# Kernel tuning notes

Hardware: AMD Instinct MI355X
Metric: run time of the kernel (lower is better)

Reference implementation:

```python
import jax, jax.numpy as jnp
import numpy as np

NEG_SLOPE = 0.01

def lrelu(x):
    return jax.nn.leaky_relu(x, NEG_SLOPE)

def lin(x, w, b):
    # torch Linear: x @ W.T + b, W shape (out, in)
    return x @ w.T + b

def meansum_pool(mask, x_local, *x_global):
    # masked sum + mean over points, concat with global/context vectors
    x_sum = (x_local * mask).sum(axis=1)                 # (b, d)
    x_mean = x_sum / mask.sum(axis=1)                    # (b, d) / (b, 1)
    return jnp.concatenate([x_mean, x_sum, *x_global], axis=1)


def setup_inputs() -> dict:
    key = jax.random.key(0)
    ks = jax.random.split(key, 16)
    B, N, DIN, DC, H, G, NB, DOUT = 16, 8192, 3, 16, 128, 10, 6, 3

    def w(k, shape, fan_in):
        return (jax.random.normal(k, shape, jnp.float32) / np.float32(np.sqrt(fan_in)))

    inp = {
        "x_local": jax.random.normal(ks[0], (B, N, DIN), jnp.float32),
        "context": jax.random.normal(ks[1], (B, DC), jnp.float32),
        "mask": (jax.random.uniform(ks[2], (B, N, 1)) < 0.9).astype(jnp.float32),
        # EPiC_Projection params (effective weight-normed weights)
        "proj_lw": w(ks[3], (H, DIN), DIN), "proj_lb": jnp.zeros((H,), jnp.float32),
        "proj_g0w": w(ks[4], (H, 2 * H + DC), 2 * H + DC), "proj_g0b": jnp.zeros((H,), jnp.float32),
        "proj_g1w": w(ks[5], (H, H), H), "proj_g1b": jnp.zeros((H,), jnp.float32),
        "proj_g2w": w(ks[6], (G, H), H), "proj_g2b": jnp.zeros((G,), jnp.float32),
        # stacked per-block EPiC_layer params
        "g1w": w(ks[7], (NB, H, 2 * H + G + DC), 2 * H + G + DC), "g1b": jnp.zeros((NB, H), jnp.float32),
        "g2w": w(ks[8], (NB, G, H), H), "g2b": jnp.zeros((NB, G), jnp.float32),
        "l1w": w(ks[9], (NB, H, H + G + DC), H + G + DC), "l1b": jnp.zeros((NB, H), jnp.float32),
        "l2w": w(ks[10], (NB, H, H), H), "l2b": jnp.zeros((NB, H), jnp.float32),
        # output head
        "outw": w(ks[11], (DOUT, H), H), "outb": jnp.zeros((DOUT,), jnp.float32),
    }
    return inp


def reference(x_local, context, mask,
              proj_lw, proj_lb, proj_g0w, proj_g0b, proj_g1w, proj_g1b, proj_g2w, proj_g2b,
              g1w, g1b, g2w, g2b, l1w, l1b, l2w, l2b, outw, outb):
    B, N, _ = x_local.shape
    # --- EPiC_Projection ---
    xl = lrelu(lin(x_local, proj_lw, proj_lb))           # (b, n, H)
    xg = meansum_pool(mask, xl, context)                 # (b, 2H + DC)
    xg = lrelu(lin(xg, proj_g0w, proj_g0b))
    xg = lrelu(lin(xg, proj_g1w, proj_g1b))
    xg = lrelu(lin(xg, proj_g2w, proj_g2b))              # (b, G)
    xl = xl * mask
    # --- EPiC layers (no skip: use_skip_connection=False -> +0) ---
    num_blocks = g1w.shape[0]
    for i in range(num_blocks):
        pooled = meansum_pool(mask, xl, xg, context)     # (b, 2H + G + DC)
        h_g = lrelu(lin(pooled, g1w[i], g1b[i]))
        xg = lrelu(lin(h_g, g2w[i], g2b[i]) + xg)        # residual global
        xg_b = jnp.broadcast_to(xg[:, None, :], (B, N, xg.shape[-1]))
        ctx_b = jnp.broadcast_to(context[:, None, :], (B, N, context.shape[-1]))
        cat = jnp.concatenate([xl, xg_b, ctx_b], axis=2)  # (b, n, H + G + DC)
        h_l = lrelu(lin(cat, l1w[i], l1b[i]))
        xl = lrelu(lin(h_l, l2w[i], l2b[i]) + xl) * mask  # residual local, masked
    h = lin(xl, outw, outb)                              # (b, n, 3)
    return h * mask
```

## Files before the change

kernel.cpp:

```cpp
#include <hip/hip_runtime.h>
#include <hip/hip_bf16.h>


typedef __attribute__((ext_vector_type(8))) short short8;
typedef __attribute__((ext_vector_type(4))) float f32x4;

#define B_ 16
#define N_ 8192
#define DC_ 16
#define H_ 128
#define G_ 10
#define NB_ 6
#define NEG_ 0.01f

__device__ __forceinline__ float lrelu(float x) { return x > 0.f ? x : NEG_ * x; }

__device__ __forceinline__ unsigned short f2bf(float x) {
  union { float f; unsigned u; } v; v.f = x;
  return (unsigned short)((v.u + 0x7fffu + ((v.u >> 16) & 1u)) >> 16);
}
__device__ __forceinline__ float bf2f(unsigned short u) {
  union { unsigned u; float f; } v; v.u = ((unsigned)u) << 16; return v.f;
}
__device__ __forceinline__ void split_bf(float x, unsigned short& h, unsigned short& l) {
  union { float f; unsigned u; } v; v.f = x;
  unsigned hu = v.u & 0xffff0000u;
  h = (unsigned short)(hu >> 16);
  union { unsigned u; float f; } hv; hv.u = hu;
  l = f2bf(x - hv.f);
}

__device__ __forceinline__ f32x4 mfma16(short8 a, short8 b, f32x4 c) {
  return __builtin_amdgcn_mfma_f32_16x16x32_bf16(a, b, c, 0, 0, 0);
}

__device__ __forceinline__ void make_frags(f32x4 v0, f32x4 v1, short8& bh, short8& bl) {
  unsigned short h, l;
#pragma unroll
  for (int j = 0; j < 4; ++j) {
    split_bf(v0[j], h, l);
    bh[j] = (short)h; bl[j] = (short)l;
  }
#pragma unroll
  for (int j = 0; j < 4; ++j) {
    split_bf(v1[j], h, l);
    bh[4 + j] = (short)h; bl[4 + j] = (short)l;
  }
}

__device__ __forceinline__ void async_cp16(const void* g, void* l) {
  __builtin_amdgcn_global_load_lds(
      (const __attribute__((address_space(1))) void*)g,
      (__attribute__((address_space(3))) void*)l, 16, 0, 0);
}

__device__ __forceinline__ void agent_store(float* p, float v) {
  __hip_atomic_store(p, v, __ATOMIC_RELAXED, __HIP_MEMORY_SCOPE_AGENT);
}
__device__ __forceinline__ float agent_load(const float* p) {
  return __hip_atomic_load(p, __ATOMIC_RELAXED, __HIP_MEMORY_SCOPE_AGENT);
}

template <int NS>
__device__ void epic_global_tail(
    int b, int tid, const float* __restrict__ pP, float cnt,
    const float* __restrict__ xg_cur, float* __restrict__ xg_next,
    const float* __restrict__ context,
    const float* __restrict__ g1w_n, const float* __restrict__ g1b_n,
    const float* __restrict__ g2w_n, const float* __restrict__ g2b_n,
    const float* __restrict__ l1w_n, const float* __restrict__ l1b_n,
    float* __restrict__ gbias_out, float* shx) {
  if (tid < 256) {
    const int f = tid & 127, kh = tid >> 7;
    const float* pr = pP + ((size_t)b * NS + kh * (NS / 2)) * 128 + f;
    float s = 0.f;
#pragma unroll 8
    for (int w = 0; w < NS / 2; ++w) s += agent_load(pr + w * 128);
    shx[tid] = s;
  }
  __syncthreads();
  if (tid < 128) {
    float s = shx[tid] + shx[tid + 128];
    shx[384 + tid] = s;
    shx[256 + tid] = s / cnt;
  }
  if (tid < G_) shx[512 + tid] = xg_cur[tid];
  if (tid >= 32 && tid < 32 + DC_) shx[522 + tid - 32] = context[b * DC_ + tid - 32];
  __syncthreads();
  if (tid < 256) {
    const int f = tid & 127, kh = tid >> 7;
    const float* wr = g1w_n + (size_t)f * 282 + kh * 142;
    const float* vp = shx + 256 + kh * 142;
    const int n2 = kh ? 70 : 71;
    float a = 0.f;
#pragma unroll 8
    for (int j = 0; j < n2; ++j) {
      float2 w2 = *(const float2*)(wr + 2 * j);
      a += w2.x * vp[2 * j] + w2.y * vp[2 * j + 1];
    }
    shx[tid] = a;
  }
  __syncthreads();
  if (tid < 128) shx[544 + tid] = lrelu(shx[tid] + shx[tid + 128] + g1b_n[tid]);
  __syncthreads();
  if (tid < G_) {
    const float* wr = g2w_n + tid * 128;
    float a = g2b_n[tid] + shx[512 + tid];
#pragma unroll 8
    for (int j = 0; j < 32; ++j) {
      float4 w4 = *(const float4*)(wr + 4 * j);
      a += w4.x * shx[544 + 4 * j] + w4.y * shx[544 + 4 * j + 1] +
           w4.z * shx[544 + 4 * j + 2] + w4.w * shx[544 + 4 * j + 3];
    }
    float v = lrelu(a);
    shx[672 + tid] = v;
    xg_next[tid] = v;
  }
  __syncthreads();
  if (tid < 128) {
    const float* wr = l1w_n + tid * 154;
    float a = l1b_n[tid];
#pragma unroll
    for (int j = 0; j < G_; ++j) a += wr[128 + j] * shx[672 + j];
#pragma unroll
    for (int j = 0; j < DC_; ++j) a += wr[138 + j] * shx[522 + j];
    gbias_out[tid] = a;
  }
}

__global__ __launch_bounds__(256) void prep_weights(
    const float* __restrict__ l1w, const float* __restrict__ l2w,
    unsigned short* __restrict__ w1h, unsigned short* __restrict__ w1l,
    unsigned short* __restrict__ w2h, unsigned short* __restrict__ w2l,
    unsigned int* __restrict__ counters) {
  int idx = blockIdx.x * 256 + threadIdx.x;
  const int total = NB_ * H_ * H_;
  if (idx < 112) counters[idx] = 0u;
  if (idx < total) {
    int i = idx / (H_ * H_), rem = idx % (H_ * H_);
    int F = rem / H_, k = rem % H_;
    int ks = k >> 5, c = k & 31;
    int mt2 = F >> 4, r2 = F & 15;
    int mt1 = ((F >> 5) << 1) | ((F >> 2) & 1);
    int r1 = (((F >> 3) & 3) << 2) | (F & 3);
    int off1 = i * 16384 + (mt1 * 4 + ks) * 512 + ((c >> 3) * 16 + r1) * 8 + (c & 7);
    int off2 = i * 16384 + (mt2 * 4 + ks) * 512 + ((c >> 3) * 16 + r2) * 8 + (c & 7);
    unsigned short h, l;
    split_bf(l1w[(i * H_ + F) * 154 + k], h, l);
    w1h[off1] = h; w1l[off1] = l;
    split_bf(l2w[(i * H_ + F) * H_ + k], h, l);
    w2h[off2] = h; w2l[off2] = l;
  }
}

__global__ __launch_bounds__(256, 2) void proj_local_kernel(
    const float* __restrict__ xloc, const float* __restrict__ maskp,
    const float* __restrict__ plw, const float* __restrict__ plb,
    float* __restrict__ xlf, float* __restrict__ pP,
    float* __restrict__ cntp, float* __restrict__ cnt_g,
    unsigned int* __restrict__ counters,
    const float* __restrict__ context,
    const float* __restrict__ g0w, const float* __restrict__ g0b,
    const float* __restrict__ g1pw, const float* __restrict__ g1pb,
    const float* __restrict__ g2pw, const float* __restrict__ g2pb,
    float* __restrict__ xg_g,
    const float* __restrict__ g1w0, const float* __restrict__ g1b0,
    const float* __restrict__ g2w0, const float* __restrict__ g2b0,
    const float* __restrict__ l1w0, const float* __restrict__ l1b0,
    float* __restrict__ gbias_g) {
  __shared__ float wq[H_][4];
  __shared__ float wsum[512];
  __shared__ float cw[4];
  __shared__ float shx[768];
  __shared__ int winflag;
  const int tid = threadIdx.x, bid = blockIdx.x;
  const int wv = tid >> 6, lane = tid & 63;
  const int q = lane >> 4, n16 = lane & 15;
  const int b = bid >> 6;
  if (tid < H_) {
    wq[tid][0] = plw[tid * 3 + 0];
    wq[tid][1] = plw[tid * 3 + 1];
    wq[tid][2] = plw[tid * 3 + 2];
    wq[tid][3] = plb[tid];
  }
  __syncthreads();
  const int t = bid * 4 + wv;
  const int p0 = t * 32;
  const int pa = p0 + n16, pb = p0 + 16 + n16;
  const float xa0 = xloc[pa * 3], xa1 = xloc[pa * 3 + 1], xa2 = xloc[pa * 3 + 2];
  const float xb0 = xloc[pb * 3], xb1 = xloc[pb * 3 + 1], xb2 = xloc[pb * 3 + 2];
  const float m0 = maskp[pa], m1 = maskp[pb];
  float* ga = xlf + (size_t)(2 * t) * 2048;
  float* gb = ga + 2048;
#pragma unroll
  for (int ms = 0; ms < 8; ++ms) {
    f32x4 v0, v1;
#pragma unroll
    for (int r = 0; r < 4; ++r) {
      const int F = ms * 16 + q * 4 + r;
      float4 w4 = *(const float4*)wq[F];
      v0[r] = lrelu(w4.x * xa0 + w4.y * xa1 + w4.z * xa2 + w4.w) * m0;
      v1[r] = lrelu(w4.x * xb0 + w4.y * xb1 + w4.z * xb2 + w4.w) * m1;
    }
    *(f32x4*)(ga + ms * 256 + (q * 16 + n16) * 4) = v0;
    *(f32x4*)(gb + ms * 256 + (q * 16 + n16) * 4) = v1;
    f32x4 s = v0 + v1;
#pragma unroll
    for (int r = 0; r < 4; ++r) {
      float sv = s[r];
      sv += __shfl_xor(sv, 1, 64);
      sv += __shfl_xor(sv, 2, 64);
      sv += __shfl_xor(sv, 4, 64);
      sv += __shfl_xor(sv, 8, 64);
      s[r] = sv;
    }
    if (n16 == 0) *(f32x4*)&wsum[wv * 128 + ms * 16 + q * 4] = s;
  }
  {
    float c = (q == 0) ? (m0 + m1) : 0.f;
    c += __shfl_xor(c, 1, 64);
    c += __shfl_xor(c, 2, 64);
    c += __shfl_xor(c, 4, 64);
    c += __shfl_xor(c, 8, 64);
    if (lane == 0) cw[wv] = c;
  }
  __syncthreads();
  if (tid < 128) {
    agent_store(&pP[(size_t)(2 * bid) * 128 + tid], wsum[tid] + wsum[128 + tid]);
    agent_store(&pP[(size_t)(2 * bid + 1) * 128 + tid], wsum[256 + tid] + wsum[384 + tid]);
  }
  if (tid == 0) agent_store(&cntp[bid], cw[0] + cw[1] + cw[2] + cw[3]);

  __syncthreads();
  if (tid == 0) winflag = (atomicAdd(&counters[b], 1u) == 63u) ? 1 : 0;
  __syncthreads();
  if (!winflag) return;
  if (tid < 64) shx[688 + tid] = agent_load(&cntp[b * 64 + tid]);
  __syncthreads();
  if (tid == 0) {
    float c = 0.f;
#pragma unroll
    for (int w = 0; w < 64; ++w) c += shx[688 + w];
    shx[752] = c;
    cnt_g[b] = c;
  }
  __syncthreads();
  const float cnt = shx[752];
  {
    const int f = tid & 127, kh = tid >> 7;
    const float* pr = pP + ((size_t)b * 128 + kh * 64) * 128 + f;
    float s = 0.f;
#pragma unroll 8
    for (int w = 0; w < 64; ++w) s += agent_load(pr + w * 128);
    shx[tid] = s;
  }
  __syncthreads();
  if (tid < 128) {
    float s = shx[tid] + shx[tid + 128];
    shx[384 + tid] = s;
    shx[256 + tid] = s / cnt;
  }
  if (tid < DC_) shx[512 + tid] = context[b * DC_ + tid];
  __syncthreads();
  {
    const int f = tid & 127, kh = tid >> 7;
    const float* wr = g0w + (size_t)f * 272 + kh * 136;
    const float* vp = shx + 256 + kh * 136;
    float a = 0.f;
#pragma unroll 8
    for (int j = 0; j < 34; ++j) {
      float4 w4 = *(const float4*)(wr + 4 * j);
      a += w4.x * vp[4 * j] + w4.y * vp[4 * j + 1] + w4.z * vp[4 * j + 2] + w4.w * vp[4 * j + 3];
    }
    __syncthreads();
    shx[tid] = a;
  }
  __syncthreads();
  if (tid < 128) shx[544 + tid] = lrelu(shx[tid] + shx[tid + 128] + g0b[tid]);
  __syncthreads();
  {
    const int f = tid & 127, kh = tid >> 7;
    const float* wr = g1pw + (size_t)f * 128 + kh * 64;
    const float* vp = shx + 544 + kh * 64;
    float a = 0.f;
#pragma unroll 8
    for (int j = 0; j < 16; ++j) {
      float4 w4 = *(const float4*)(wr + 4 * j);
      a += w4.x * vp[4 * j] + w4.y * vp[4 * j + 1] + w4.z * vp[4 * j + 2] + w4.w * vp[4 * j + 3];
    }
    __syncthreads();
    shx[tid] = a;
  }
  __syncthreads();
  if (tid < 128) shx[544 + tid] = lrelu(shx[tid] + shx[tid + 128] + g1pb[tid]);
  __syncthreads();
  if (tid < G_) {
    const float* wr = g2pw + tid * 128;
    float a = g2pb[tid];
#pragma unroll 8
    for (int j = 0; j < 32; ++j) {
      float4 w4 = *(const float4*)(wr + 4 * j);
      a += w4.x * shx[544 + 4 * j] + w4.y * shx[544 + 4 * j + 1] +
           w4.z * shx[544 + 4 * j + 2] + w4.w * shx[544 + 4 * j + 3];
    }
    xg_g[(0 * 16 + b) * 16 + tid] = lrelu(a);
  }
  __syncthreads();
  epic_global_tail<128>(b, tid, pP, cnt,
                        xg_g + (0 * 16 + b) * 16, xg_g + (1 * 16 + b) * 16, context,
                        g1w0, g1b0, g2w0, g2b0, l1w0, l1b0,
                        gbias_g + (size_t)(0 * 16 + b) * 128, shx);
}

__device__ __forceinline__ void load_frags(const float* base_g, int q, int n16,
                                           short8* xbh, short8* xbl) {
#pragma unroll
  for (int ks = 0; ks < 4; ++ks) {
    const float* pb = base_g + (2 * ks + (q >> 1)) * 256 + ((q & 1) * 32 + n16) * 4;
    f32x4 v0 = *(const f32x4*)pb;
    f32x4 v1 = *(const f32x4*)(pb + 64);
    make_frags(v0, v1, xbh[ks], xbl[ks]);
  }
}

template <bool LAST>
__device__ __forceinline__ void epic_pass(
    int g, int wv, int q, int n16, int lane16,
    const short8* xbh, const short8* xbl,
    const unsigned short* w1h_l, const unsigned short* w1l_l,
    const unsigned short* w2h_l, const unsigned short* w2l_l,
    const float* gbias_s, const float* l2b_s, const float* outw_s,
    float* wsum, float* __restrict__ xlf, const float* __restrict__ maskp,
    float* __restrict__ outp) {
  f32x4 acc2[8];
#pragma unroll
  for (int ms = 0; ms < 8; ++ms) acc2[ms] = (f32x4){0.f, 0.f, 0.f, 0.f};

#pragma unroll 1
  for (int ko = 0; ko < 4; ++ko) {
    f32x4 acc[2][2];
#pragma unroll
    for (int t = 0; t < 2; ++t)
#pragma unroll
      for (int kc = 0; kc < 2; ++kc) acc[t][kc] = (f32x4){0.f, 0.f, 0.f, 0.f};
#pragma unroll
    for (int t = 0; t < 2; ++t) {
#pragma unroll
      for (int kc = 0; kc < 2; ++kc) {
        short8 a1h[2], a1l[2];
#pragma unroll
        for (int u = 0; u < 2; ++u) {
          const int off = ((ko * 2 + t) * 4 + kc * 2 + u) * 512 + lane16;
          a1h[u] = *(const short8*)(w1h_l + off);
          a1l[u] = *(const short8*)(w1l_l + off);
        }
#pragma unroll
        for (int u = 0; u < 2; ++u) {
          const int ks = kc * 2 + u;
          acc[t][kc] = mfma16(a1h[u], xbh[ks], acc[t][kc]);
          acc[t][kc] = mfma16(a1l[u], xbh[ks], acc[t][kc]);
          acc[t][kc] = mfma16(a1h[u], xbl[ks], acc[t][kc]);
        }
      }
    }
    f32x4 gb0 = *(const f32x4*)&gbias_s[ko * 32 + q * 8];
    f32x4 gb1 = *(const f32x4*)&gbias_s[ko * 32 + q * 8 + 4];
    f32x4 hv0, hv1;
#pragma unroll
    for (int r = 0; r < 4; ++r) {
      hv0[r] = lrelu(acc[0][0][r] + acc[0][1][r] + gb0[r]);
      hv1[r] = lrelu(acc[1][0][r] + acc[1][1][r] + gb1[r]);
    }
    short8 b2h, b2l;
    make_frags(hv0, hv1, b2h, b2l);
#pragma unroll
    for (int mc = 0; mc < 4; ++mc) {
      short8 a2h[2], a2l[2];
#pragma unroll
      for (int u = 0; u < 2; ++u) {
        const int off = ((mc * 2 + u) * 4 + ko) * 512 + lane16;
        a2h[u] = *(const short8*)(w2h_l + off);
        a2l[u] = *(const short8*)(w2l_l + off);
      }
#pragma unroll
      for (int u = 0; u < 2; ++u) {
        const int ms = mc * 2 + u;
        acc2[ms] = mfma16(a2h[u], b2h, acc2[ms]);
        acc2[ms] = mfma16(a2l[u], b2h, acc2[ms]);
        acc2[ms] = mfma16(a2h[u], b2l, acc2[ms]);
      }
    }
  }

  const float mk = maskp[g * 16 + n16];
  float po[3];
  if (LAST) po[0] = po[1] = po[2] = 0.f;
  float* base_w = xlf + (size_t)g * 2048;
#pragma unroll
  for (int ms = 0; ms < 8; ++ms) {
    f32x4 lb4 = *(const f32x4*)&l2b_s[ms * 16 + q * 4];
    float* xo = base_w + ms * 256 + (q * 16 + n16) * 4;
    f32x4 old = *(const f32x4*)xo;
    f32x4 v;
#pragma unroll
    for (int r = 0; r < 4; ++r) v[r] = lrelu(acc2[ms][r] + lb4[r] + old[r]) * mk;
    if (!LAST) {
      *(f32x4*)xo = v;
      f32x4 sr;
#pragma unroll
      for (int r = 0; r < 4; ++r) {
        float s = v[r];
        s += __shfl_xor(s, 1, 64);
        s += __shfl_xor(s, 2, 64);
        s += __shfl_xor(s, 4, 64);
        s += __shfl_xor(s, 8, 64);
        sr[r] = s;
      }
      if (n16 == 0) *(f32x4*)&wsum[wv * 128 + ms * 16 + q * 4] = sr;
    } else {
      f32x4 w0 = *(const f32x4*)&outw_s[0 * 128 + ms * 16 + q * 4];
      f32x4 w1 = *(const f32x4*)&outw_s[1 * 128 + ms * 16 + q * 4];
      f32x4 w2 = *(const f32x4*)&outw_s[2 * 128 + ms * 16 + q * 4];
#pragma unroll
      for (int r = 0; r < 4; ++r) {
        po[0] += v[r] * w0[r];
        po[1] += v[r] * w1[r];
        po[2] += v[r] * w2[r];
      }
    }
  }
  if (LAST) {
#pragma unroll
    for (int o = 0; o < 3; ++o) {
      float s = po[o];
      s += __shfl_xor(s, 16, 64);
      s += __shfl_xor(s, 32, 64);
      po[o] = s;
    }
    if (q == 0) {
      const int p = g * 16 + n16;
#pragma unroll
      for (int o = 0; o < 3; ++o)
        outp[(size_t)p * 3 + o] = (po[o] + outw_s[384 + o]) * mk;
    }
  }
}

__global__ __launch_bounds__(1024) void epic_local_kernel(
    float* __restrict__ xlf, float* __restrict__ pP,
    const float* __restrict__ cnt_g, unsigned int* __restrict__ counters_blk,
    const float* __restrict__ gbias_in,
    const float* __restrict__ xg_tail_cur, float* __restrict__ xg_tail_next,
    float* __restrict__ gbias_tail_out,
    const float* __restrict__ context,
    const float* __restrict__ g1w_n, const float* __restrict__ g1b_n,
    const float* __restrict__ g2w_n, const float* __restrict__ g2b_n,
    const float* __restrict__ l1w_n, const float* __restrict__ l1b_n,
    const float* __restrict__ l2b,
    const unsigned short* __restrict__ w1h, const unsigned short* __restrict__ w1l,
    const unsigned short* __restrict__ w2h, const unsigned short* __restrict__ w2l,
    const float* __restrict__ maskp,
    float* __restrict__ outp) {
  __shared__ unsigned short wbuf[65536];
  __shared__ float shx[768];
  __shared__ float gbias_s[128];
  __shared__ float l2b_s[128];
  __shared__ float wsum[2048];
  __shared__ int winflag;
  const int tid = threadIdx.x, bid = blockIdx.x;
  const int b = bid >> 4;
  const int wv = tid >> 6, lane = tid & 63;
  const int q = lane >> 4, n16 = lane & 15;

  {
    const unsigned short* src =
        (wv < 4) ? w1h : (wv < 8) ? w1l : (wv < 12) ? w2h : w2l;
    const char* s8 = (const char*)(src + (wv & 3) * 4096) + lane * 16;
    char* d8 = (char*)wbuf + wv * 8192;
#pragma unroll
    for (int j = 0; j < 8; ++j) async_cp16(s8 + j * 1024, d8 + j * 1024);
  }
  if (tid < 128) {
    gbias_s[tid] = gbias_in[b * 128 + tid];
    l2b_s[tid] = l2b[tid];
  }

  const int gA = bid * 32 + wv;
  const int gB = bid * 32 + 16 + wv;
  short8 xbh[4], xbl[4];
  load_frags(xlf + (size_t)gA * 2048, q, n16, xbh, xbl);
  __syncthreads();

  const unsigned short* w1h_l = wbuf;
  const unsigned short* w1l_l = wbuf + 16384;
  const unsigned short* w2h_l = wbuf + 32768;
  const unsigned short* w2l_l = wbuf + 49152;
  const int lane16 = lane * 8;

  epic_pass<false>(gA, wv, q, n16, lane16, xbh, xbl, w1h_l, w1l_l, w2h_l, w2l_l,
                   gbias_s, l2b_s, nullptr, wsum, xlf, maskp, outp);
  __syncthreads();
  if (tid < 128) {
    float s = 0.f;
#pragma unroll
    for (int w = 0; w < 16; ++w) s += wsum[w * 128 + tid];
    agent_store(&pP[(size_t)(bid * 2) * 128 + tid], s);
  }
  __syncthreads();

  load_frags(xlf + (size_t)gB * 2048, q, n16, xbh, xbl);
  epic_pass<false>(gB, wv, q, n16, lane16, xbh, xbl, w1h_l, w1l_l, w2h_l, w2l_l,
                   gbias_s, l2b_s, nullptr, wsum, xlf, maskp, outp);
  __syncthreads();
  if (tid < 128) {
    float s = 0.f;
#pragma unroll
    for (int w = 0; w < 16; ++w) s += wsum[w * 128 + tid];
    agent_store(&pP[(size_t)(bid * 2 + 1) * 128 + tid], s);
  }

  __syncthreads();
  if (tid == 0) winflag = (atomicAdd(&counters_blk[b], 1u) == 15u) ? 1 : 0;
  __syncthreads();
  if (!winflag) return;
  epic_global_tail<32>(b, tid, pP, cnt_g[b], xg_tail_cur + b * 16, xg_tail_next + b * 16,
                       context, g1w_n, g1b_n, g2w_n, g2b_n, l1w_n, l1b_n,
                       gbias_tail_out + (size_t)b * 128, shx);
}

__global__ __launch_bounds__(512, 2) void epic_last_kernel(
    const float* __restrict__ xlf,
    const float* __restrict__ gbias_in,
    const float* __restrict__ l2b,
    const unsigned short* __restrict__ w1h, const unsigned short* __restrict__ w1l,
    const unsigned short* __restrict__ w2h, const unsigned short* __restrict__ w2l,
    const float* __restrict__ maskp,
    const float* __restrict__ outw, const float* __restrict__ outb,
    float* __restrict__ outp) {
  __shared__ unsigned short wbuf[65536];
  __shared__ float gbias_s[128];
  __shared__ float l2b_s[128];
  __shared__ float outw_s[392];
  const int tid = threadIdx.x, bid = blockIdx.x;
  const int b = bid >> 4;
  const int wv = tid >> 6, lane = tid & 63;
  const int q = lane >> 4, n16 = lane & 15;
  const int lane16 = lane * 8;

  {
    const unsigned short* src =
        (wv < 2) ? w1h : (wv < 4) ? w1l : (wv < 6) ? w2h : w2l;
    const char* s8 = (const char*)(src + (wv & 1) * 8192) + lane * 16;
    char* d8 = (char*)wbuf + wv * 16384;
#pragma unroll
    for (int j = 0; j < 16; ++j) async_cp16(s8 + j * 1024, d8 + j * 1024);
  }
  if (tid < 128) {
    gbias_s[tid] = gbias_in[b * 128 + tid];
    l2b_s[tid] = l2b[tid];
  }
  if (tid < 384) outw_s[tid] = outw[tid];
  if (tid >= 384 && tid < 387) outw_s[tid] = outb[tid - 384];
  __syncthreads();

  const unsigned short* w1h_l = wbuf;
  const unsigned short* w1l_l = wbuf + 16384;
  const unsigned short* w2h_l = wbuf + 32768;
  const unsigned short* w2l_l = wbuf + 49152;

#pragma unroll 1
  for (int p4 = 0; p4 < 4; ++p4) {
    const int g = bid * 32 + wv * 4 + p4;
    short8 xbh[4], xbl[4];
    load_frags(xlf + (size_t)g * 2048, q, n16, xbh, xbl);
    epic_pass<true>(g, wv, q, n16, lane16, xbh, xbl, w1h_l, w1l_l, w2h_l, w2l_l,
                    gbias_s, l2b_s, outw_s, gbias_s ,
                    const_cast<float*>(xlf), maskp, outp);
  }
}

extern "C" void kernel_launch(void* const* d_in, const int* in_sizes, int n_in,
                              void* d_out, int out_size, void* d_ws, size_t ws_size,
                              hipStream_t stream) {
  const float* x_local = (const float*)d_in[0];
  const float* context = (const float*)d_in[1];
  const float* mask = (const float*)d_in[2];
  const float* proj_lw = (const float*)d_in[3];
  const float* proj_lb = (const float*)d_in[4];
  const float* proj_g0w = (const float*)d_in[5];
  const float* proj_g0b = (const float*)d_in[6];
  const float* proj_g1w = (const float*)d_in[7];
  const float* proj_g1b = (const float*)d_in[8];
  const float* proj_g2w = (const float*)d_in[9];
  const float* proj_g2b = (const float*)d_in[10];
  const float* g1w = (const float*)d_in[11];
  const float* g1b = (const float*)d_in[12];
  const float* g2w = (const float*)d_in[13];
  const float* g2b = (const float*)d_in[14];
  const float* l1w = (const float*)d_in[15];
  const float* l1b = (const float*)d_in[16];
  const float* l2w = (const float*)d_in[17];
  const float* l2b = (const float*)d_in[18];
  const float* outw = (const float*)d_in[19];
  const float* outb = (const float*)d_in[20];
  float* out = (float*)d_out;

  char* ws = (char*)d_ws;
  float* xlf = (float*)ws;
  float* pP = (float*)(ws + 67108864);
  float* cntp = (float*)(ws + 68157440);
  float* cnt_g = (float*)(ws + 68161536);
  float* xg_g = (float*)(ws + 68161600);
  float* gbias_g = (float*)(ws + 68168768);
  unsigned int* counters = (unsigned int*)(ws + 68217920);
  unsigned short* w1h = (unsigned short*)(ws + 68218368);
  unsigned short* w1l = (unsigned short*)(ws + 68414976);
  unsigned short* w2h = (unsigned short*)(ws + 68611584);
  unsigned short* w2l = (unsigned short*)(ws + 68808192);

  prep_weights<<<384, 256, 0, stream>>>(l1w, l2w, w1h, w1l, w2h, w2l, counters);
  proj_local_kernel<<<1024, 256, 0, stream>>>(
      x_local, mask, proj_lw, proj_lb, xlf, pP, cntp, cnt_g, counters, context,
      proj_g0w, proj_g0b, proj_g1w, proj_g1b, proj_g2w, proj_g2b, xg_g,
      g1w, g1b, g2w, g2b, l1w, l1b, gbias_g);
  for (int i = 0; i < NB_; ++i) {
    const int j = i + 1;
    const float* g1w_n = g1w + (size_t)j * 128 * 282;
    const float* g1b_n = g1b + j * 128;
    const float* g2w_n = g2w + j * 10 * 128;
    const float* g2b_n = g2b + j * 10;
    const float* l1w_n = l1w + (size_t)j * 128 * 154;
    const float* l1b_n = l1b + j * 128;
    const unsigned short* w1h_i = w1h + i * 16384;
    const unsigned short* w1l_i = w1l + i * 16384;
    const unsigned short* w2h_i = w2h + i * 16384;
    const unsigned short* w2l_i = w2l + i * 16384;
    if (i == NB_ - 1) {
      epic_last_kernel<<<256, 512, 0, stream>>>(
          xlf, gbias_g + (size_t)(i * 16) * 128, l2b + i * 128,
          w1h_i, w1l_i, w2h_i, w2l_i, mask, outw, outb, out);
    } else {
      epic_local_kernel<<<256, 1024, 0, stream>>>(
          xlf, pP, cnt_g, counters + (i + 1) * 16, gbias_g + (size_t)(i * 16) * 128,
          xg_g + (i + 1) * 16 * 16, xg_g + (i + 2) * 16 * 16,
          gbias_g + (size_t)((i + 1) * 16) * 128, context,
          g1w_n, g1b_n, g2w_n, g2b_n, l1w_n, l1b_n,
          l2b + i * 128, w1h_i, w1l_i, w2h_i, w2l_i, mask, out);
    }
  }
}
```

Baseline: 447.0 us.

## Process two point groups per wave in local kernel; prefetch next-block tail weights

The per-block local kernel now runs 512 threads with 2 blocks per CU. Each wave handles four 16-point groups, two at a time, so every weight fragment read from LDS feeds MFMAs for two groups. The masked-sum reduction now accumulates per-wave rows instead of being reduced twice with extra barriers. Designated blocks also touch the next layer's global-tail weights (g1w, l1w, g2w) early so they are warm in cache when the winning block runs the tail. The trade-off is higher register pressure from doubled accumulators and fewer waves per block.

```diff
diff --git a/kernel.cpp b/kernel.cpp
--- a/kernel.cpp
+++ b/kernel.cpp
@@ -177,6 +177,19 @@
   const int wv = tid >> 6, lane = tid & 63;
   const int q = lane >> 4, n16 = lane & 15;
   const int b = bid >> 6;
+
+  float pfacc = 0.f;
+  if ((bid & 31) == 0) {
+    const int ch = bid >> 5;
+    const int t0 = ch * 256 + tid, STR = 32 * 256;
+    const float4* p;
+    p = (const float4*)g0w;  for (int i = t0; i < 8704; i += STR) pfacc += p[i].x;
+    p = (const float4*)g1pw; for (int i = t0; i < 4096; i += STR) pfacc += p[i].x;
+    p = (const float4*)g1w0; for (int i = t0; i < 9024; i += STR) pfacc += p[i].x;
+    p = (const float4*)l1w0; for (int i = t0; i < 4928; i += STR) pfacc += p[i].x;
+    if (t0 < 320) pfacc += ((const float4*)g2pw)[t0].x + ((const float4*)g2w0)[t0].x;
+  }
+
   if (tid < H_) {
     wq[tid][0] = plw[tid * 3 + 0];
     wq[tid][1] = plw[tid * 3 + 1];
@@ -230,6 +243,7 @@
     agent_store(&pP[(size_t)(2 * bid + 1) * 128 + tid], wsum[256 + tid] + wsum[384 + tid]);
   }
   if (tid == 0) agent_store(&cntp[bid], cw[0] + cw[1] + cw[2] + cw[3]);
+  asm volatile("" :: "v"(pfacc));
 
   __syncthreads();
   if (tid == 0) winflag = (atomicAdd(&counters[b], 1u) == 63u) ? 1 : 0;
@@ -320,6 +334,117 @@
     f32x4 v0 = *(const f32x4*)pb;
     f32x4 v1 = *(const f32x4*)(pb + 64);
     make_frags(v0, v1, xbh[ks], xbl[ks]);
+  }
+}
+
+__device__ __forceinline__ void pair_pass2(
+    int g0i, int q, int n16, int lane16,
+    const short8 (&xh)[2][4], const short8 (&xl)[2][4],
+    const unsigned short* w1h_l, const unsigned short* w1l_l,
+    const unsigned short* w2h_l, const unsigned short* w2l_l,
+    const float* gbias_s, const float* l2b_s,
+    float* wsum_row, float* __restrict__ xlf, const float* __restrict__ maskp) {
+  f32x4 acc2[2][8];
+#pragma unroll
+  for (int g = 0; g < 2; ++g)
+#pragma unroll
+    for (int ms = 0; ms < 8; ++ms) acc2[g][ms] = (f32x4){0.f, 0.f, 0.f, 0.f};
+
+#pragma unroll 1
+  for (int ko = 0; ko < 4; ++ko) {
+    f32x4 acc[2][2];
+#pragma unroll
+    for (int g = 0; g < 2; ++g)
+#pragma unroll
+      for (int t = 0; t < 2; ++t) acc[g][t] = (f32x4){0.f, 0.f, 0.f, 0.f};
+#pragma unroll
+    for (int t = 0; t < 2; ++t) {
+#pragma unroll
+      for (int kc = 0; kc < 2; ++kc) {
+        short8 a1h[2], a1l[2];
+#pragma unroll
+        for (int u = 0; u < 2; ++u) {
+          const int off = ((ko * 2 + t) * 4 + kc * 2 + u) * 512 + lane16;
+          a1h[u] = *(const short8*)(w1h_l + off);
+          a1l[u] = *(const short8*)(w1l_l + off);
+        }
+#pragma unroll
+        for (int u = 0; u < 2; ++u) {
+          const int ks = kc * 2 + u;
+          acc[0][t] = mfma16(a1h[u], xh[0][ks], acc[0][t]);
+          acc[0][t] = mfma16(a1l[u], xh[0][ks], acc[0][t]);
+          acc[0][t] = mfma16(a1h[u], xl[0][ks], acc[0][t]);
+          acc[1][t] = mfma16(a1h[u], xh[1][ks], acc[1][t]);
+          acc[1][t] = mfma16(a1l[u], xh[1][ks], acc[1][t]);
+          acc[1][t] = mfma16(a1h[u], xl[1][ks], acc[1][t]);
+        }
+      }
+    }
+    f32x4 gb0 = *(const f32x4*)&gbias_s[ko * 32 + q * 8];
+    f32x4 gb1 = *(const f32x4*)&gbias_s[ko * 32 + q * 8 + 4];
+    short8 b2h[2], b2l[2];
+#pragma unroll
+    for (int g = 0; g < 2; ++g) {
+      f32x4 hv0, hv1;
+#pragma unroll
+      for (int r = 0; r < 4; ++r) {
+        hv0[r] = lrelu(acc[g][0][r] + gb0[r]);
+        hv1[r] = lrelu(acc[g][1][r] + gb1[r]);
+      }
+      make_frags(hv0, hv1, b2h[g], b2l[g]);
+    }
+#pragma unroll
+    for (int mc = 0; mc < 4; ++mc) {
+      short8 a2h[2], a2l[2];
+#pragma unroll
+      for (int u = 0; u < 2; ++u) {
+        const int off = ((mc * 2 + u) * 4 + ko) * 512 + lane16;
+        a2h[u] = *(const short8*)(w2h_l + off);
+        a2l[u] = *(const short8*)(w2l_l + off);
+      }
+#pragma unroll
+      for (int u = 0; u < 2; ++u) {
+        const int ms = mc * 2 + u;
+        acc2[0][ms] = mfma16(a2h[u], b2h[0], acc2[0][ms]);
+        acc2[0][ms] = mfma16(a2l[u], b2h[0], acc2[0][ms]);
+        acc2[0][ms] = mfma16(a2h[u], b2l[0], acc2[0][ms]);
+        acc2[1][ms] = mfma16(a2h[u], b2h[1], acc2[1][ms]);
+        acc2[1][ms] = mfma16(a2l[u], b2h[1], acc2[1][ms]);
+        acc2[1][ms] = mfma16(a2h[u], b2l[1], acc2[1][ms]);
+      }
+    }
+  }
+
+#pragma unroll
+  for (int g = 0; g < 2; ++g) {
+    const int grp = g0i + g;
+    const float mk = maskp[grp * 16 + n16];
+    float* base_w = xlf + (size_t)grp * 2048;
+#pragma unroll
+    for (int ms = 0; ms < 8; ++ms) {
+      f32x4 lb4 = *(const f32x4*)&l2b_s[ms * 16 + q * 4];
+      float* xo = base_w + ms * 256 + (q * 16 + n16) * 4;
+      f32x4 old = *(const f32x4*)xo;
+      f32x4 v;
+#pragma unroll
+      for (int r = 0; r < 4; ++r) v[r] = lrelu(acc2[g][ms][r] + lb4[r] + old[r]) * mk;
+      *(f32x4*)xo = v;
+      f32x4 sr;
+#pragma unroll
+      for (int r = 0; r < 4; ++r) {
+        float s = v[r];
+        s += __shfl_xor(s, 1, 64);
+        s += __shfl_xor(s, 2, 64);
+        s += __shfl_xor(s, 4, 64);
+        s += __shfl_xor(s, 8, 64);
+        sr[r] = s;
+      }
+      if (n16 == 0) {
+        f32x4 tcur = *(const f32x4*)&wsum_row[ms * 16 + q * 4];
+        tcur += sr;
+        *(f32x4*)&wsum_row[ms * 16 + q * 4] = tcur;
+      }
+    }
   }
 }
 
@@ -446,7 +571,7 @@
   }
 }
 
-__global__ __launch_bounds__(1024) void epic_local_kernel(
+__global__ __launch_bounds__(512, 2) void epic_local_kernel(
     float* __restrict__ xlf, float* __restrict__ pP,
     const float* __restrict__ cnt_g, unsigned int* __restrict__ counters_blk,
     const float* __restrict__ gbias_in,
@@ -465,58 +590,66 @@
   __shared__ float shx[768];
   __shared__ float gbias_s[128];
   __shared__ float l2b_s[128];
-  __shared__ float wsum[2048];
+  __shared__ float wsum[1024];
   __shared__ int winflag;
   const int tid = threadIdx.x, bid = blockIdx.x;
   const int b = bid >> 4;
   const int wv = tid >> 6, lane = tid & 63;
   const int q = lane >> 4, n16 = lane & 15;
+  const int lane16 = lane * 8;
+
+  float pfacc = 0.f;
+  if ((bid & 15) == 0) {
+    const int ch = bid >> 4;
+    const int t0 = ch * 512 + tid, STR = 16 * 512;
+    const float4* p;
+    p = (const float4*)g1w_n; for (int i = t0; i < 9024; i += STR) pfacc += p[i].x;
+    p = (const float4*)l1w_n; for (int i = t0; i < 4928; i += STR) pfacc += p[i].x;
+    if (t0 < 320) pfacc += ((const float4*)g2w_n)[t0].x;
+  }
 
   {
     const unsigned short* src =
-        (wv < 4) ? w1h : (wv < 8) ? w1l : (wv < 12) ? w2h : w2l;
-    const char* s8 = (const char*)(src + (wv & 3) * 4096) + lane * 16;
-    char* d8 = (char*)wbuf + wv * 8192;
-#pragma unroll
-    for (int j = 0; j < 8; ++j) async_cp16(s8 + j * 1024, d8 + j * 1024);
+        (wv < 2) ? w1h : (wv < 4) ? w1l : (wv < 6) ? w2h : w2l;
+    const char* s8 = (const char*)(src + (wv & 1) * 8192) + lane * 16;
+    char* d8 = (char*)wbuf + wv * 16384;
+#pragma unroll
+    for (int j = 0; j < 16; ++j) async_cp16(s8 + j * 1024, d8 + j * 1024);
   }
   if (tid < 128) {
     gbias_s[tid] = gbias_in[b * 128 + tid];
     l2b_s[tid] = l2b[tid];
   }
-
-  const int gA = bid * 32 + wv;
-  const int gB = bid * 32 + 16 + wv;
-  short8 xbh[4], xbl[4];
-  load_frags(xlf + (size_t)gA * 2048, q, n16, xbh, xbl);
+  if (lane < 32) *(f32x4*)&wsum[wv * 128 + lane * 4] = (f32x4){0.f, 0.f, 0.f, 0.f};
+
+  const int g0 = bid * 32 + wv * 4;
+  short8 xh[2][4], xl2[2][4];
+  load_frags(xlf + (size_t)g0 * 2048, q, n16, xh[0], xl2[0]);
+  load_frags(xlf + (size_t)(g0 + 1) * 2048, q, n16, xh[1], xl2[1]);
   __syncthreads();
 
   const unsigned short* w1h_l = wbuf;
   const unsigned short* w1l_l = wbuf + 16384;
   const unsigned short* w2h_l = wbuf + 32768;
   const unsigned short* w2l_l = wbuf + 49152;
-  const int lane16 = lane * 8;
-
-  epic_pass<false>(gA, wv, q, n16, lane16, xbh, xbl, w1h_l, w1l_l, w2h_l, w2l_l,
-                   gbias_s, l2b_s, nullptr, wsum, xlf, maskp, outp);
+
+  pair_pass2(g0, q, n16, lane16, xh, xl2, w1h_l, w1l_l, w2h_l, w2l_l,
+             gbias_s, l2b_s, &wsum[wv * 128], xlf, maskp);
+  asm volatile("" :: "v"(pfacc));
+
+  load_frags(xlf + (size_t)(g0 + 2) * 2048, q, n16, xh[0], xl2[0]);
+  load_frags(xlf + (size_t)(g0 + 3) * 2048, q, n16, xh[1], xl2[1]);
+  pair_pass2(g0 + 2, q, n16, lane16, xh, xl2, w1h_l, w1l_l, w2h_l, w2l_l,
+             gbias_s, l2b_s, &wsum[wv * 128], xlf, maskp);
+
   __syncthreads();
   if (tid < 128) {
-    float s = 0.f;
-#pragma unroll
-    for (int w = 0; w < 16; ++w) s += wsum[w * 128 + tid];
-    agent_store(&pP[(size_t)(bid * 2) * 128 + tid], s);
-  }
-  __syncthreads();
-
-  load_frags(xlf + (size_t)gB * 2048, q, n16, xbh, xbl);
-  epic_pass<false>(gB, wv, q, n16, lane16, xbh, xbl, w1h_l, w1l_l, w2h_l, w2l_l,
-                   gbias_s, l2b_s, nullptr, wsum, xlf, maskp, outp);
-  __syncthreads();
-  if (tid < 128) {
-    float s = 0.f;
-#pragma unroll
-    for (int w = 0; w < 16; ++w) s += wsum[w * 128 + tid];
-    agent_store(&pP[(size_t)(bid * 2 + 1) * 128 + tid], s);
+    float sA = wsum[0 * 128 + tid] + wsum[1 * 128 + tid] +
+               wsum[2 * 128 + tid] + wsum[3 * 128 + tid];
+    float sB = wsum[4 * 128 + tid] + wsum[5 * 128 + tid] +
+               wsum[6 * 128 + tid] + wsum[7 * 128 + tid];
+    agent_store(&pP[(size_t)(bid * 2) * 128 + tid], sA);
+    agent_store(&pP[(size_t)(bid * 2 + 1) * 128 + tid], sB);
   }
 
   __syncthreads();
@@ -640,7 +773,7 @@
           xlf, gbias_g + (size_t)(i * 16) * 128, l2b + i * 128,
           w1h_i, w1l_i, w2h_i, w2l_i, mask, outw, outb, out);
     } else {
-      epic_local_kernel<<<256, 1024, 0, stream>>>(
+      epic_local_kernel<<<256, 512, 0, stream>>>(
           xlf, pP, cnt_g, counters + (i + 1) * 16, gbias_g + (size_t)(i * 16) * 128,
           xg_g + (i + 1) * 16 * 16, xg_g + (i + 2) * 16 * 16,
           gbias_g + (size_t)((i + 1) * 16) * 128, context,
```

New measurement: 467.8 us. 1.05x slower.

## Replace last-block atomic global tails with redundant per-block prologue recompute

Applied to the files above, without the earlier changes.

Removes the atomic-counter last-block pattern, where one block per batch computed the global MLP and gbias after all others finished. Instead, every block of the next kernel recomputes the pooled global path (and, for the first layer, the projection MLP) in a prologue before its local pass. Partial sums are ping-ponged between two buffers. This drops the serialized tail and the counter atomics, at the cost of redundant global work in every block, whose prologue now delays the local matmuls.

```diff
diff --git a/kernel.cpp b/kernel.cpp
--- a/kernel.cpp
+++ b/kernel.cpp
@@ -128,14 +128,107 @@
   }
 }
 
+template <bool FIRST, int NS>
+__device__ void epic_prologue(
+    int b, int tid, int layer,
+    const float* __restrict__ pP_in, const float* __restrict__ cntp,
+    const float* __restrict__ context, float* __restrict__ xg_g,
+    const float* __restrict__ g1w_i, const float* __restrict__ g1b_i,
+    const float* __restrict__ g2w_i, const float* __restrict__ g2b_i,
+    const float* __restrict__ l1w_i, const float* __restrict__ l1b_i,
+    const float* __restrict__ g0w, const float* __restrict__ g0b,
+    const float* __restrict__ g1pw, const float* __restrict__ g1pb,
+    const float* __restrict__ g2pw, const float* __restrict__ g2pb,
+    float* gbias_s, float* shx) {
+  if (tid < 64) shx[688 + tid] = agent_load(&cntp[b * 64 + tid]);
+  __syncthreads();
+  if (tid == 0) {
+    float c = 0.f;
+#pragma unroll
+    for (int w = 0; w < 64; ++w) c += shx[688 + w];
+    shx[752] = c;
+  }
+  __syncthreads();
+  const float cnt = shx[752];
+
+  if (FIRST) {
+    if (tid < 256) {
+      const int f = tid & 127, kh = tid >> 7;
+      const float* pr = pP_in + ((size_t)b * 128 + kh * 64) * 128 + f;
+      float s = 0.f;
+#pragma unroll 8
+      for (int w = 0; w < 64; ++w) s += agent_load(pr + w * 128);
+      shx[tid] = s;
+    }
+    __syncthreads();
+    if (tid < 128) {
+      float s = shx[tid] + shx[tid + 128];
+      shx[384 + tid] = s;
+      shx[256 + tid] = s / cnt;
+    }
+    if (tid < DC_) shx[512 + tid] = context[b * DC_ + tid];
+    __syncthreads();
+    {
+      float a = 0.f;
+      if (tid < 256) {
+        const int f = tid & 127, kh = tid >> 7;
+        const float* wr = g0w + (size_t)f * 272 + kh * 136;
+        const float* vp = shx + 256 + kh * 136;
+#pragma unroll 8
+        for (int j = 0; j < 34; ++j) {
+          float4 w4 = *(const float4*)(wr + 4 * j);
+          a += w4.x * vp[4 * j] + w4.y * vp[4 * j + 1] + w4.z * vp[4 * j + 2] + w4.w * vp[4 * j + 3];
+        }
+      }
+      __syncthreads();
+      if (tid < 256) shx[tid] = a;
+    }
+    __syncthreads();
+    if (tid < 128) shx[544 + tid] = lrelu(shx[tid] + shx[tid + 128] + g0b[tid]);
+    __syncthreads();
+    {
+      float a = 0.f;
+      if (tid < 256) {
+        const int f = tid & 127, kh = tid >> 7;
+        const float* wr = g1pw + (size_t)f * 128 + kh * 64;
+        const float* vp = shx + 544 + kh * 64;
+#pragma unroll 8
+        for (int j = 0; j < 16; ++j) {
+          float4 w4 = *(const float4*)(wr + 4 * j);
+          a += w4.x * vp[4 * j] + w4.y * vp[4 * j + 1] + w4.z * vp[4 * j + 2] + w4.w * vp[4 * j + 3];
+        }
+      }
+      __syncthreads();
+      if (tid < 256) shx[tid] = a;
+    }
+    __syncthreads();
+    if (tid < 128) shx[544 + tid] = lrelu(shx[tid] + shx[tid + 128] + g1pb[tid]);
+    __syncthreads();
+    if (tid < G_) {
+      const float* wr = g2pw + tid * 128;
+      float a = g2pb[tid];
+#pragma unroll 8
+      for (int j = 0; j < 32; ++j) {
+        float4 w4 = *(const float4*)(wr + 4 * j);
+        a += w4.x * shx[544 + 4 * j] + w4.y * shx[544 + 4 * j + 1] +
+             w4.z * shx[544 + 4 * j + 2] + w4.w * shx[544 + 4 * j + 3];
+      }
+      xg_g[(0 * 16 + b) * 16 + tid] = lrelu(a);
+    }
+    __syncthreads();
+  }
+  epic_global_tail<NS>(b, tid, pP_in, cnt,
+                       xg_g + ((size_t)layer * 16 + b) * 16,
+                       xg_g + ((size_t)(layer + 1) * 16 + b) * 16, context,
+                       g1w_i, g1b_i, g2w_i, g2b_i, l1w_i, l1b_i, gbias_s, shx);
+}
+
 __global__ __launch_bounds__(256) void prep_weights(
     const float* __restrict__ l1w, const float* __restrict__ l2w,
     unsigned short* __restrict__ w1h, unsigned short* __restrict__ w1l,
-    unsigned short* __restrict__ w2h, unsigned short* __restrict__ w2l,
-    unsigned int* __restrict__ counters) {
+    unsigned short* __restrict__ w2h, unsigned short* __restrict__ w2l) {
   int idx = blockIdx.x * 256 + threadIdx.x;
   const int total = NB_ * H_ * H_;
-  if (idx < 112) counters[idx] = 0u;
   if (idx < total) {
     int i = idx / (H_ * H_), rem = idx % (H_ * H_);
     int F = rem / H_, k = rem % H_;
@@ -157,26 +250,13 @@
     const float* __restrict__ xloc, const float* __restrict__ maskp,
     const float* __restrict__ plw, const float* __restrict__ plb,
     float* __restrict__ xlf, float* __restrict__ pP,
-    float* __restrict__ cntp, float* __restrict__ cnt_g,
-    unsigned int* __restrict__ counters,
-    const float* __restrict__ context,
-    const float* __restrict__ g0w, const float* __restrict__ g0b,
-    const float* __restrict__ g1pw, const float* __restrict__ g1pb,
-    const float* __restrict__ g2pw, const float* __restrict__ g2pb,
-    float* __restrict__ xg_g,
-    const float* __restrict__ g1w0, const float* __restrict__ g1b0,
-    const float* __restrict__ g2w0, const float* __restrict__ g2b0,
-    const float* __restrict__ l1w0, const float* __restrict__ l1b0,
-    float* __restrict__ gbias_g) {
+    float* __restrict__ cntp) {
   __shared__ float wq[H_][4];
   __shared__ float wsum[512];
   __shared__ float cw[4];
-  __shared__ float shx[768];
-  __shared__ int winflag;
   const int tid = threadIdx.x, bid = blockIdx.x;
   const int wv = tid >> 6, lane = tid & 63;
   const int q = lane >> 4, n16 = lane & 15;
-  const int b = bid >> 6;
   if (tid < H_) {
     wq[tid][0] = plw[tid * 3 + 0];
     wq[tid][1] = plw[tid * 3 + 1];
@@ -230,86 +310,6 @@
     agent_store(&pP[(size_t)(2 * bid + 1) * 128 + tid], wsum[256 + tid] + wsum[384 + tid]);
   }
   if (tid == 0) agent_store(&cntp[bid], cw[0] + cw[1] + cw[2] + cw[3]);
-
-  __syncthreads();
-  if (tid == 0) winflag = (atomicAdd(&counters[b], 1u) == 63u) ? 1 : 0;
-  __syncthreads();
-  if (!winflag) return;
-  if (tid < 64) shx[688 + tid] = agent_load(&cntp[b * 64 + tid]);
-  __syncthreads();
-  if (tid == 0) {
-    float c = 0.f;
-#pragma unroll
-    for (int w = 0; w < 64; ++w) c += shx[688 + w];
-    shx[752] = c;
-    cnt_g[b] = c;
-  }
-  __syncthreads();
-  const float cnt = shx[752];
-  {
-    const int f = tid & 127, kh = tid >> 7;
-    const float* pr = pP + ((size_t)b * 128 + kh * 64) * 128 + f;
-    float s = 0.f;
-#pragma unroll 8
-    for (int w = 0; w < 64; ++w) s += agent_load(pr + w * 128);
-    shx[tid] = s;
-  }
-  __syncthreads();
-  if (tid < 128) {
-    float s = shx[tid] + shx[tid + 128];
-    shx[384 + tid] = s;
-    shx[256 + tid] = s / cnt;
-  }
-  if (tid < DC_) shx[512 + tid] = context[b * DC_ + tid];
-  __syncthreads();
-  {
-    const int f = tid & 127, kh = tid >> 7;
-    const float* wr = g0w + (size_t)f * 272 + kh * 136;
-    const float* vp = shx + 256 + kh * 136;
-    float a = 0.f;
-#pragma unroll 8
-    for (int j = 0; j < 34; ++j) {
-      float4 w4 = *(const float4*)(wr + 4 * j);
-      a += w4.x * vp[4 * j] + w4.y * vp[4 * j + 1] + w4.z * vp[4 * j + 2] + w4.w * vp[4 * j + 3];
-    }
-    __syncthreads();
-    shx[tid] = a;
-  }
-  __syncthreads();
-  if (tid < 128) shx[544 + tid] = lrelu(shx[tid] + shx[tid + 128] + g0b[tid]);
-  __syncthreads();
-  {
-    const int f = tid & 127, kh = tid >> 7;
-    const float* wr = g1pw + (size_t)f * 128 + kh * 64;
-    const float* vp = shx + 544 + kh * 64;
-    float a = 0.f;
-#pragma unroll 8
-    for (int j = 0; j < 16; ++j) {
-      float4 w4 = *(const float4*)(wr + 4 * j);
-      a += w4.x * vp[4 * j] + w4.y * vp[4 * j + 1] + w4.z * vp[4 * j + 2] + w4.w * vp[4 * j + 3];
-    }
-    __syncthreads();
-    shx[tid] = a;
-  }
-  __syncthreads();
-  if (tid < 128) shx[544 + tid] = lrelu(shx[tid] + shx[tid + 128] + g1pb[tid]);
-  __syncthreads();
-  if (tid < G_) {
-    const float* wr = g2pw + tid * 128;
-    float a = g2pb[tid];
-#pragma unroll 8
-    for (int j = 0; j < 32; ++j) {
-      float4 w4 = *(const float4*)(wr + 4 * j);
-      a += w4.x * shx[544 + 4 * j] + w4.y * shx[544 + 4 * j + 1] +
-           w4.z * shx[544 + 4 * j + 2] + w4.w * shx[544 + 4 * j + 3];
-    }
-    xg_g[(0 * 16 + b) * 16 + tid] = lrelu(a);
-  }
-  __syncthreads();
-  epic_global_tail<128>(b, tid, pP, cnt,
-                        xg_g + (0 * 16 + b) * 16, xg_g + (1 * 16 + b) * 16, context,
-                        g1w0, g1b0, g2w0, g2b0, l1w0, l1b0,
-                        gbias_g + (size_t)(0 * 16 + b) * 128, shx);
 }
 
 __device__ __forceinline__ void load_frags(const float* base_g, int q, int n16,
@@ -446,27 +446,27 @@
   }
 }
 
+template <bool FIRST>
 __global__ __launch_bounds__(1024) void epic_local_kernel(
-    float* __restrict__ xlf, float* __restrict__ pP,
-    const float* __restrict__ cnt_g, unsigned int* __restrict__ counters_blk,
-    const float* __restrict__ gbias_in,
-    const float* __restrict__ xg_tail_cur, float* __restrict__ xg_tail_next,
-    float* __restrict__ gbias_tail_out,
-    const float* __restrict__ context,
-    const float* __restrict__ g1w_n, const float* __restrict__ g1b_n,
-    const float* __restrict__ g2w_n, const float* __restrict__ g2b_n,
-    const float* __restrict__ l1w_n, const float* __restrict__ l1b_n,
+    float* __restrict__ xlf,
+    const float* __restrict__ pP_in, float* __restrict__ pP_out,
+    const float* __restrict__ cntp, const float* __restrict__ context,
+    float* __restrict__ xg_g, int layer,
+    const float* __restrict__ g1w_i, const float* __restrict__ g1b_i,
+    const float* __restrict__ g2w_i, const float* __restrict__ g2b_i,
+    const float* __restrict__ l1w_i, const float* __restrict__ l1b_i,
+    const float* __restrict__ g0w, const float* __restrict__ g0b,
+    const float* __restrict__ g1pw, const float* __restrict__ g1pb,
+    const float* __restrict__ g2pw, const float* __restrict__ g2pb,
     const float* __restrict__ l2b,
     const unsigned short* __restrict__ w1h, const unsigned short* __restrict__ w1l,
     const unsigned short* __restrict__ w2h, const unsigned short* __restrict__ w2l,
-    const float* __restrict__ maskp,
-    float* __restrict__ outp) {
+    const float* __restrict__ maskp) {
   __shared__ unsigned short wbuf[65536];
   __shared__ float shx[768];
   __shared__ float gbias_s[128];
   __shared__ float l2b_s[128];
   __shared__ float wsum[2048];
-  __shared__ int winflag;
   const int tid = threadIdx.x, bid = blockIdx.x;
   const int b = bid >> 4;
   const int wv = tid >> 6, lane = tid & 63;
@@ -480,16 +480,18 @@
 #pragma unroll
     for (int j = 0; j < 8; ++j) async_cp16(s8 + j * 1024, d8 + j * 1024);
   }
-  if (tid < 128) {
-    gbias_s[tid] = gbias_in[b * 128 + tid];
-    l2b_s[tid] = l2b[tid];
-  }
+  if (tid < 128) l2b_s[tid] = l2b[tid];
+
+  epic_prologue<FIRST, FIRST ? 128 : 32>(
+      b, tid, layer, pP_in, cntp, context, xg_g,
+      g1w_i, g1b_i, g2w_i, g2b_i, l1w_i, l1b_i,
+      g0w, g0b, g1pw, g1pb, g2pw, g2pb, gbias_s, shx);
+  __syncthreads();
 
   const int gA = bid * 32 + wv;
   const int gB = bid * 32 + 16 + wv;
   short8 xbh[4], xbl[4];
   load_frags(xlf + (size_t)gA * 2048, q, n16, xbh, xbl);
-  __syncthreads();
 
   const unsigned short* w1h_l = wbuf;
   const unsigned short* w1l_l = wbuf + 16384;
@@ -498,39 +500,35 @@
   const int lane16 = lane * 8;
 
   epic_pass<false>(gA, wv, q, n16, lane16, xbh, xbl, w1h_l, w1l_l, w2h_l, w2l_l,
-                   gbias_s, l2b_s, nullptr, wsum, xlf, maskp, outp);
+                   gbias_s, l2b_s, nullptr, wsum, xlf, maskp, nullptr);
   __syncthreads();
   if (tid < 128) {
     float s = 0.f;
 #pragma unroll
     for (int w = 0; w < 16; ++w) s += wsum[w * 128 + tid];
-    agent_store(&pP[(size_t)(bid * 2) * 128 + tid], s);
+    agent_store(&pP_out[(size_t)(bid * 2) * 128 + tid], s);
   }
   __syncthreads();
 
   load_frags(xlf + (size_t)gB * 2048, q, n16, xbh, xbl);
   epic_pass<false>(gB, wv, q, n16, lane16, xbh, xbl, w1h_l, w1l_l, w2h_l, w2l_l,
-                   gbias_s, l2b_s, nullptr, wsum, xlf, maskp, outp);
+                   gbias_s, l2b_s, nullptr, wsum, xlf, maskp, nullptr);
   __syncthreads();
   if (tid < 128) {
     float s = 0.f;
 #pragma unroll
     for (int w = 0; w < 16; ++w) s += wsum[w * 128 + tid];
-    agent_store(&pP[(size_t)(bid * 2 + 1) * 128 + tid], s);
-  }
-
-  __syncthreads();
-  if (tid == 0) winflag = (atomicAdd(&counters_blk[b], 1u) == 15u) ? 1 : 0;
-  __syncthreads();
-  if (!winflag) return;
-  epic_global_tail<32>(b, tid, pP, cnt_g[b], xg_tail_cur + b * 16, xg_tail_next + b * 16,
-                       context, g1w_n, g1b_n, g2w_n, g2b_n, l1w_n, l1b_n,
-                       gbias_tail_out + (size_t)b * 128, shx);
+    agent_store(&pP_out[(size_t)(bid * 2 + 1) * 128 + tid], s);
+  }
 }
 
 __global__ __launch_bounds__(512, 2) void epic_last_kernel(
     const float* __restrict__ xlf,
-    const float* __restrict__ gbias_in,
+    const float* __restrict__ pP_in, const float* __restrict__ cntp,
+    const float* __restrict__ context, float* __restrict__ xg_g,
+    const float* __restrict__ g1w_i, const float* __restrict__ g1b_i,
+    const float* __restrict__ g2w_i, const float* __restrict__ g2b_i,
+    const float* __restrict__ l1w_i, const float* __restrict__ l1b_i,
     const float* __restrict__ l2b,
     const unsigned short* __restrict__ w1h, const unsigned short* __restrict__ w1l,
     const unsigned short* __restrict__ w2h, const unsigned short* __restrict__ w2l,
@@ -538,6 +536,7 @@
     const float* __restrict__ outw, const float* __restrict__ outb,
     float* __restrict__ outp) {
   __shared__ unsigned short wbuf[65536];
+  __shared__ float shx[768];
   __shared__ float gbias_s[128];
   __shared__ float l2b_s[128];
   __shared__ float outw_s[392];
@@ -555,12 +554,14 @@
 #pragma unroll
     for (int j = 0; j < 16; ++j) async_cp16(s8 + j * 1024, d8 + j * 1024);
   }
-  if (tid < 128) {
-    gbias_s[tid] = gbias_in[b * 128 + tid];
-    l2b_s[tid] = l2b[tid];
-  }
+  if (tid < 128) l2b_s[tid] = l2b[tid];
   if (tid < 384) outw_s[tid] = outw[tid];
   if (tid >= 384 && tid < 387) outw_s[tid] = outb[tid - 384];
+
+  epic_prologue<false, 32>(
+      b, tid, 5, pP_in, cntp, context, xg_g,
+      g1w_i, g1b_i, g2w_i, g2b_i, l1w_i, l1b_i,
+      nullptr, nullptr, nullptr, nullptr, nullptr, nullptr, gbias_s, shx);
   __syncthreads();
 
   const unsigned short* w1h_l = wbuf;
@@ -609,43 +610,52 @@
   float* xlf = (float*)ws;
   float* pP = (float*)(ws + 67108864);
   float* cntp = (float*)(ws + 68157440);
-  float* cnt_g = (float*)(ws + 68161536);
   float* xg_g = (float*)(ws + 68161600);
-  float* gbias_g = (float*)(ws + 68168768);
-  unsigned int* counters = (unsigned int*)(ws + 68217920);
   unsigned short* w1h = (unsigned short*)(ws + 68218368);
   unsigned short* w1l = (unsigned short*)(ws + 68414976);
   unsigned short* w2h = (unsigned short*)(ws + 68611584);
   unsigned short* w2l = (unsigned short*)(ws + 68808192);
-
-  prep_weights<<<384, 256, 0, stream>>>(l1w, l2w, w1h, w1l, w2h, w2l, counters);
+  float* pPe0 = (float*)(ws + 69004800);
+  float* pPe1 = (float*)(ws + 69266944);
+
+  prep_weights<<<384, 256, 0, stream>>>(l1w, l2w, w1h, w1l, w2h, w2l);
   proj_local_kernel<<<1024, 256, 0, stream>>>(
-      x_local, mask, proj_lw, proj_lb, xlf, pP, cntp, cnt_g, counters, context,
-      proj_g0w, proj_g0b, proj_g1w, proj_g1b, proj_g2w, proj_g2b, xg_g,
-      g1w, g1b, g2w, g2b, l1w, l1b, gbias_g);
-  for (int i = 0; i < NB_; ++i) {
-    const int j = i + 1;
-    const float* g1w_n = g1w + (size_t)j * 128 * 282;
-    const float* g1b_n = g1b + j * 128;
-    const float* g2w_n = g2w + j * 10 * 128;
-    const float* g2b_n = g2b + j * 10;
-    const float* l1w_n = l1w + (size_t)j * 128 * 154;
-    const float* l1b_n = l1b + j * 128;
+      x_local, mask, proj_lw, proj_lb, xlf, pP, cntp);
+  for (int i = 0; i < NB_ - 1; ++i) {
+    const float* pP_in = (i == 0) ? pP : ((i & 1) ? pPe1 : pPe0);
+    float* pP_out = ((i + 1) & 1) ? pPe1 : pPe0;
+    const float* g1w_i = g1w + (size_t)i * 128 * 282;
+    const float* g1b_i = g1b + i * 128;
+    const float* g2w_i = g2w + (size_t)i * 10 * 128;
+    const float* g2b_i = g2b + i * 10;
+    const float* l1w_i = l1w + (size_t)i * 128 * 154;
+    const float* l1b_i = l1b + i * 128;
     const unsigned short* w1h_i = w1h + i * 16384;
     const unsigned short* w1l_i = w1l + i * 16384;
     const unsigned short* w2h_i = w2h + i * 16384;
     const unsigned short* w2l_i = w2l + i * 16384;
-    if (i == NB_ - 1) {
-      epic_last_kernel<<<256, 512, 0, stream>>>(
-          xlf, gbias_g + (size_t)(i * 16) * 128, l2b + i * 128,
-          w1h_i, w1l_i, w2h_i, w2l_i, mask, outw, outb, out);
+    if (i == 0) {
+      epic_local_kernel<true><<<256, 1024, 0, stream>>>(
+          xlf, pP_in, pP_out, cntp, context, xg_g, i,
+          g1w_i, g1b_i, g2w_i, g2b_i, l1w_i, l1b_i,
+          proj_g0w, proj_g0b, proj_g1w, proj_g1b, proj_g2w, proj_g2b,
+          l2b + i * 128, w1h_i, w1l_i, w2h_i, w2l_i, mask);
     } else {
-      epic_local_kernel<<<256, 1024, 0, stream>>>(
-          xlf, pP, cnt_g, counters + (i + 1) * 16, gbias_g + (size_t)(i * 16) * 128,
-          xg_g + (i + 1) * 16 * 16, xg_g + (i + 2) * 16 * 16,
-          gbias_g + (size_t)((i + 1) * 16) * 128, context,
-          g1w_n, g1b_n, g2w_n, g2b_n, l1w_n, l1b_n,
-          l2b + i * 128, w1h_i, w1l_i, w2h_i, w2l_i, mask, out);
-    }
-  }
-}
+      epic_local_kernel<false><<<256, 1024, 0, stream>>>(
+          xlf, pP_in, pP_out, cntp, context, xg_g, i,
+          g1w_i, g1b_i, g2w_i, g2b_i, l1w_i, l1b_i,
+          nullptr, nullptr, nullptr, nullptr, nullptr, nullptr,
+          l2b + i * 128, w1h_i, w1l_i, w2h_i, w2l_i, mask);
+    }
+  }
+  {
+    const int i = NB_ - 1;
+    epic_last_kernel<<<256, 512, 0, stream>>>(
+        xlf, pPe1 , cntp, context, xg_g,
+        g1w + (size_t)i * 128 * 282, g1b + i * 128,
+        g2w + (size_t)i * 10 * 128, g2b + i * 10,
+        l1w + (size_t)i * 128 * 154, l1b + i * 128,
+        l2b + i * 128, w1h + i * 16384, w1l + i * 16384,
+        w2h + i * 16384, w2l + i * 16384, mask, outw, outb, out);
+  }
+}
```

Measured after the change: 413.2 us. 7.6% less time.
